# Kernel optimization log

Hardware: AMD Instinct MI355X
Metric: run time of the kernel (lower is better)

## Reference

```python
import jax, jax.numpy as jnp
import numpy as np

SCALE = 8
NUM_CLASSES = 15
IGNORE_THRES = 0.5
# anchors for scale=8 divided by scale
GRID_ANCHOR = jnp.array([[96.0 / 8, 230.0 / 8], [79.0 / 8, 186.0 / 8], [81.0 / 8, 133.0 / 8]], dtype=jnp.float32)  # [3,2]


def _bce_sum(p, t, mask):
    # torch BCELoss(reduction='sum') with log clamped at -100, restricted to mask
    lp = jnp.maximum(jnp.log(p), -100.0)
    ln = jnp.maximum(jnp.log(1.0 - p), -100.0)
    return jnp.sum(-(t * lp + (1.0 - t) * ln) * mask)


def setup_inputs() -> dict:
    key = jax.random.key(0)
    k1, k2, k3 = jax.random.split(key, 3)
    nB, nG = 128, 52
    x = jax.random.normal(k1, (nB, 3 * (NUM_CLASSES + 5), nG, nG), dtype=jnp.float32)
    boxes = jax.random.uniform(k2, (nB, 4), minval=0.1, maxval=0.6)  # cx,cy,w,h in (0,1)
    cls = jax.random.randint(k3, (nB, 1), 0, NUM_CLASSES).astype(jnp.float32)
    labels = jnp.concatenate([boxes, cls], axis=-1)  # [nB,5]
    return {"x": x, "labels": labels}


def reference(x, labels):
    nB, nG = x.shape[0], x.shape[2]
    pred = x.reshape(nB, 3, NUM_CLASSES + 5, nG, nG).transpose(0, 1, 3, 4, 2)  # [B,3,G,G,20]
    px = jax.nn.sigmoid(pred[..., 0])
    py = jax.nn.sigmoid(pred[..., 1])
    pw = pred[..., 2]
    ph = pred[..., 3]
    conf = jax.nn.sigmoid(pred[..., 4])
    cls = jax.nn.softmax(pred[..., 5:], axis=-1)
    pred_boxs = jnp.stack([px, py, pw, ph], axis=-1)  # [B,3,G,G,4]
    out = jnp.concatenate([
        pred_boxs.reshape(nB, -1, 4) * SCALE,
        conf.reshape(nB, -1, 1),
        cls.reshape(nB, -1, NUM_CLASSES),
    ], axis=-1)

    # ---- build_targets (vectorized; one target per image as in original loop) ----
    tb = labels[:, :4] * nG  # boxes in grid units [B,4]
    gx, gy, gw, gh = tb[:, 0], tb[:, 1], tb[:, 2], tb[:, 3]
    gi = gx.astype(jnp.int32)
    gj = gy.astype(jnp.int32)
    gcls = labels[:, 4].astype(jnp.int32)

    # wh-IoU anchors vs targets -> [3,B]
    aw, ah = GRID_ANCHOR[:, 0:1], GRID_ANCHOR[:, 1:2]
    inter_wh = jnp.minimum(aw, gw[None, :]) * jnp.minimum(ah, gh[None, :])
    ious = inter_wh / (aw * ah + 1e-16 + gw[None, :] * gh[None, :] - inter_wh)
    best_idx = jnp.argmax(ious, axis=0)  # [B]

    bidx = jnp.arange(nB)
    shape4 = (nB, 3, nG, nG)
    obj = jnp.zeros(shape4, jnp.float32).at[bidx, best_idx, gj, gi].set(1.0)

    noobj = jnp.ones(shape4, jnp.float32)
    arep = jnp.tile(jnp.arange(3), nB)
    brep = jnp.repeat(bidx, 3)
    jrep = jnp.repeat(gj, 3)
    irep = jnp.repeat(gi, 3)
    ign = (jnp.reshape(ious.T, (-1,)) > IGNORE_THRES).astype(jnp.float32)
    noobj = noobj.at[brep, arep, jrep, irep].mul(1.0 - ign)
    noobj = noobj.at[bidx, best_idx, gj, gi].set(0.0)

    gif = gi.astype(jnp.float32)
    gjf = gj.astype(jnp.float32)
    tx = jnp.zeros(shape4, jnp.float32).at[bidx, best_idx, gj, gi].set(gx - gif)
    ty = jnp.zeros(shape4, jnp.float32).at[bidx, best_idx, gj, gi].set(gy - gjf)
    tw = jnp.zeros(shape4, jnp.float32).at[bidx, best_idx, gj, gi].set(jnp.log(gw / GRID_ANCHOR[best_idx, 0] + 1e-16))
    th = jnp.zeros(shape4, jnp.float32).at[bidx, best_idx, gj, gi].set(jnp.log(gh / GRID_ANCHOR[best_idx, 1] + 1e-16))
    tcls = jnp.zeros(shape4 + (NUM_CLASSES,), jnp.float32).at[bidx, best_idx, gj, gi, gcls].set(1.0)

    # cls_mask: does argmax of predicted class at target cell match gt class
    pred_cls_at = cls[bidx, best_idx, gj, gi]  # [B,15]
    cls_hit = (jnp.argmax(pred_cls_at, axis=-1) == gcls).astype(jnp.float32)
    cls_mask = jnp.zeros(shape4, jnp.float32).at[bidx, best_idx, gj, gi].set(cls_hit)

    # iou between pred box at target cell and target box (cxcywh, +1 corner convention)
    pb = pred_boxs[bidx, best_idx, gj, gi]  # [B,4]
    b1x1, b1y1 = pb[:, 0] - pb[:, 2] / 2, pb[:, 1] - pb[:, 3] / 2
    b1x2, b1y2 = pb[:, 0] + pb[:, 2] / 2, pb[:, 1] + pb[:, 3] / 2
    b2x1, b2y1 = gx - gw / 2, gy - gh / 2
    b2x2, b2y2 = gx + gw / 2, gy + gh / 2
    iw = jnp.clip(jnp.minimum(b1x2, b2x2) - jnp.maximum(b1x1, b2x1) + 1, 0)
    ih = jnp.clip(jnp.minimum(b1y2, b2y2) - jnp.maximum(b1y1, b2y1) + 1, 0)
    inter = iw * ih
    a1 = (b1x2 - b1x1 + 1) * (b1y2 - b1y1 + 1)
    a2 = (b2x2 - b2x1 + 1) * (b2y2 - b2y1 + 1)
    iou_vec = inter / (a1 + a2 - inter + 1e-16)
    iou_scores = jnp.zeros(shape4, jnp.float32).at[bidx, best_idx, gj, gi].set(iou_vec)

    tconf = obj
    # ---- losses (boolean-mask indexing replaced by masked sums) ----
    loss_x = jnp.sum(jnp.abs(px - tx) * obj)
    loss_y = jnp.sum(jnp.abs(py - ty) * obj)
    loss_w = jnp.sum(jnp.abs(pw - tw) * obj)
    loss_h = jnp.sum(jnp.abs(ph - th) * obj)
    loss_conf = _bce_sum(conf, tconf, obj) + 100.0 * _bce_sum(conf, tconf, noobj)
    loss_cls = _bce_sum(cls, tcls, obj[..., None])
    loss = loss_x + loss_y + loss_w + loss_h + loss_conf + loss_cls
    return (loss, out)
```

## Files before the change

kernel.cpp:

```cpp
#include <hip/hip_runtime.h>
#include <math.h>

#define NB    128
#define NG    52
#define NGG   2704
#define NA    3
#define NCLS  15
#define NCH   20
#define NQ    8112
#define TOTAL 1038336
#define BLK   256
#define CPT   2
#define CPB   (BLK*CPT)
#define NBLK  (TOTAL/CPB)
#define FPB   (CPB*NCH)
#define NQUAD ((FPB-4)/4)

__global__ __launch_bounds__(BLK) void main_kernel(const float* __restrict__ x,
                                                   float* __restrict__ out,
                                                   float* __restrict__ partials) {
    __shared__ __align__(16) float sm[FPB];
    __shared__ float wred[BLK/64];

    int t = threadIdx.x;
    int g = blockIdx.x * BLK + t;
    int cell0 = g * CPT;
    int b  = cell0 / NQ;
    int r  = cell0 - b * NQ;
    int a  = r / NGG;
    int ji = r - a * NGG;

    const float2* __restrict__ xp =
        (const float2*)(x + ((size_t)(b*60 + a*20)) * NGG) + (ji >> 1);

    float za[NCH], zb[NCH];
    #pragma unroll
    for (int c = 0; c < NCH; c++) {
        float2 zz = xp[c * (NGG/2)];
        za[c] = zz.x; zb[c] = zz.y;
    }

    float tsum = 0.0f;
    #pragma unroll
    for (int i = 0; i < CPT; i++) {
        const float* z = (i == 0) ? za : zb;
        float v[NCH];
        float conf = 1.0f / (1.0f + expf(-z[4]));
        v[0] = 8.0f / (1.0f + expf(-z[0]));
        v[1] = 8.0f / (1.0f + expf(-z[1]));
        v[2] = 8.0f * z[2];
        v[3] = 8.0f * z[3];
        v[4] = conf;
        float m = z[5];
        #pragma unroll
        for (int c = 6; c < NCH; c++) m = fmaxf(m, z[c]);
        float s = 0.0f;
        #pragma unroll
        for (int c = 0; c < NCLS; c++) { v[5+c] = expf(z[5+c] - m); s += v[5+c]; }
        float inv = 1.0f / s;
        #pragma unroll
        for (int c = 0; c < NCLS; c++) v[5+c] *= inv;

        tsum += -fmaxf(logf(1.0f - conf), -100.0f);

        int cl = (t * CPT + i);
        int base = cl * NCH - 3;
        #pragma unroll
        for (int c = 0; c < NCH; c++) {
            int L = base + c;
            if (L < 0) L += FPB;
            sm[L] = v[c];
        }
    }

    #pragma unroll
    for (int off = 32; off > 0; off >>= 1) tsum += __shfl_down(tsum, off, 64);
    if ((t & 63) == 0) wred[t >> 6] = tsum;

    __syncthreads();

    size_t gbase = (size_t)blockIdx.x * FPB;
    float4* __restrict__ op = (float4*)(out + gbase + 4);
    const float4* __restrict__ sp = (const float4*)sm;
    #pragma unroll
    for (int k = 0; k < 10; k++) {
        int q = k * BLK + t;
        if (q < NQUAD) op[q] = sp[q];
    }
    if (t == 0) {
        out[gbase + 1]    = sm[FPB - 3];
        out[gbase + 2]    = sm[FPB - 2];
        out[gbase + 3]    = sm[FPB - 1];
        out[gbase + FPB]  = sm[FPB - 4];
        partials[blockIdx.x] = wred[0] + wred[1] + wred[2] + wred[3];
    }
}

__global__ void finish_kernel(const float* __restrict__ labels,
                              const float* __restrict__ partials,
                              float* __restrict__ out) {
    int t = threadIdx.x;
    float s = 0.0f;
    for (int q = t; q < NBLK; q += 256) s += partials[q];

    float corr_part = 0.0f;
    if (t < NB) {
        int b = t;
        float gx = labels[b*5+0] * (float)NG;
        float gy = labels[b*5+1] * (float)NG;
        float gw = labels[b*5+2] * (float)NG;
        float gh = labels[b*5+3] * (float)NG;
        int gcls = (int)labels[b*5+4];
        int gi = (int)gx, gj = (int)gy;
        const float aw[3] = {12.0f, 9.875f, 10.125f};
        const float ah[3] = {28.75f, 23.25f, 16.625f};
        float iou[3];
        #pragma unroll
        for (int a = 0; a < 3; a++) {
            float inter = fminf(aw[a], gw) * fminf(ah[a], gh);
            iou[a] = inter / (aw[a]*ah[a] + 1e-16f + gw*gh - inter);
        }
        int best = 0; float bv = iou[0];
        if (iou[1] > bv) { best = 1; bv = iou[1]; }
        if (iou[2] > bv) { best = 2; bv = iou[2]; }
        float txv = gx - (float)gi;
        float tyv = gy - (float)gj;
        float twv = logf(gw / aw[best] + 1e-16f);
        float thv = logf(gh / ah[best] + 1e-16f);

        float corr = 0.0f;
        #pragma unroll
        for (int a = 0; a < 3; a++) {
            int q = a*NGG + gj*NG + gi;
            const float* ob = out + 1 + ((size_t)b*NQ + q) * NCH;
            float conf = ob[4];
            bool isbest = (a == best);
            if (isbest || iou[a] > 0.5f) {
                corr += -fmaxf(logf(1.0f - conf), -100.0f);
            }
            if (isbest) {
                corr_part += -fmaxf(logf(conf), -100.0f);
                float px = ob[0]*0.125f, py = ob[1]*0.125f;
                float pw = ob[2]*0.125f, ph = ob[3]*0.125f;
                corr_part += fabsf(px - txv) + fabsf(py - tyv)
                           + fabsf(pw - twv) + fabsf(ph - thv);
                for (int c = 0; c < NCLS; c++) {
                    float p = ob[5 + c];
                    if (c == gcls) corr_part += -fmaxf(logf(p),        -100.0f);
                    else           corr_part += -fmaxf(logf(1.0f - p), -100.0f);
                }
            }
        }
        corr_part -= 100.0f * corr;
    }

    __shared__ float red[256];
    red[t] = 100.0f * s + corr_part;
    __syncthreads();
    for (int s2 = 128; s2 > 0; s2 >>= 1) {
        if (t < s2) red[t] += red[t + s2];
        __syncthreads();
    }
    if (t == 0) out[0] = red[0];
}

extern "C" void kernel_launch(void* const* d_in, const int* in_sizes, int n_in,
                              void* d_out, int out_size, void* d_ws, size_t ws_size,
                              hipStream_t stream) {
    const float* x      = (const float*)d_in[0];
    const float* labels = (const float*)d_in[1];
    float* out = (float*)d_out;
    float* ws  = (float*)d_ws;

    hipLaunchKernelGGL(main_kernel,   dim3(NBLK), dim3(BLK), 0, stream, x, out, ws);
    hipLaunchKernelGGL(finish_kernel, dim3(1),    dim3(256), 0, stream, labels, ws, out);
}
```

Measured before the change: 157.3 us.

## Write output directly from registers using lane shuffles instead of LDS staging

```diff
diff --git a/kernel.cpp b/kernel.cpp
--- a/kernel.cpp
+++ b/kernel.cpp
@@ -10,21 +10,18 @@
 #define NQ    8112
 #define TOTAL 1038336
 #define BLK   256
-#define CPT   2
-#define CPB   (BLK*CPT)
-#define NBLK  (TOTAL/CPB)
-#define FPB   (CPB*NCH)
-#define NQUAD ((FPB-4)/4)
+#define NTHREADS (TOTAL/2)
+#define NBLK  (NTHREADS/BLK)
+#define NPART (NBLK*4)
+
+__device__ __forceinline__ float sigmoidf(float z) { return 1.0f / (1.0f + expf(-z)); }
 
 __global__ __launch_bounds__(BLK) void main_kernel(const float* __restrict__ x,
                                                    float* __restrict__ out,
                                                    float* __restrict__ partials) {
-    __shared__ __align__(16) float sm[FPB];
-    __shared__ float wred[BLK/64];
-
     int t = threadIdx.x;
-    int g = blockIdx.x * BLK + t;
-    int cell0 = g * CPT;
+    int T = blockIdx.x * BLK + t;
+    int cell0 = T * 2;
     int b  = cell0 / NQ;
     int r  = cell0 - b * NQ;
     int a  = r / NGG;
@@ -40,60 +37,82 @@
         za[c] = zz.x; zb[c] = zz.y;
     }
 
-    float tsum = 0.0f;
-    #pragma unroll
-    for (int i = 0; i < CPT; i++) {
-        const float* z = (i == 0) ? za : zb;
-        float v[NCH];
-        float conf = 1.0f / (1.0f + expf(-z[4]));
-        v[0] = 8.0f / (1.0f + expf(-z[0]));
-        v[1] = 8.0f / (1.0f + expf(-z[1]));
-        v[2] = 8.0f * z[2];
-        v[3] = 8.0f * z[3];
-        v[4] = conf;
-        float m = z[5];
+    float w[40];
+    float tsum;
+
+    float va0 = 8.0f * sigmoidf(za[0]);
+    float va1 = 8.0f * sigmoidf(za[1]);
+    float va2 = 8.0f * za[2];
+    w[0] = 8.0f * za[3];
+    {
+        float conf = sigmoidf(za[4]);
+        w[1] = conf;
+        tsum = -fmaxf(logf(1.0f - conf), -100.0f);
+        float m = za[5];
         #pragma unroll
-        for (int c = 6; c < NCH; c++) m = fmaxf(m, z[c]);
+        for (int c = 6; c < NCH; c++) m = fmaxf(m, za[c]);
         float s = 0.0f;
         #pragma unroll
-        for (int c = 0; c < NCLS; c++) { v[5+c] = expf(z[5+c] - m); s += v[5+c]; }
+        for (int c = 0; c < NCLS; c++) { w[2+c] = expf(za[5+c] - m); s += w[2+c]; }
         float inv = 1.0f / s;
         #pragma unroll
-        for (int c = 0; c < NCLS; c++) v[5+c] *= inv;
+        for (int c = 0; c < NCLS; c++) w[2+c] *= inv;
+    }
 
+    w[17] = 8.0f * sigmoidf(zb[0]);
+    w[18] = 8.0f * sigmoidf(zb[1]);
+    w[19] = 8.0f * zb[2];
+    w[20] = 8.0f * zb[3];
+    {
+        float conf = sigmoidf(zb[4]);
+        w[21] = conf;
         tsum += -fmaxf(logf(1.0f - conf), -100.0f);
+        float m = zb[5];
+        #pragma unroll
+        for (int c = 6; c < NCH; c++) m = fmaxf(m, zb[c]);
+        float s = 0.0f;
+        #pragma unroll
+        for (int c = 0; c < NCLS; c++) { w[22+c] = expf(zb[5+c] - m); s += w[22+c]; }
+        float inv = 1.0f / s;
+        #pragma unroll
+        for (int c = 0; c < NCLS; c++) w[22+c] *= inv;
+    }
 
-        int cl = (t * CPT + i);
-        int base = cl * NCH - 3;
-        #pragma unroll
-        for (int c = 0; c < NCH; c++) {
-            int L = base + c;
-            if (L < 0) L += FPB;
-            sm[L] = v[c];
+    w[37] = __shfl_down(va0, 1, 64);
+    w[38] = __shfl_down(va1, 1, 64);
+    w[39] = __shfl_down(va2, 1, 64);
+    if ((t & 63) == 63) {
+        int cell2 = cell0 + 2;
+        if (cell2 < TOTAL) {
+            int b2  = cell2 / NQ;
+            int r2  = cell2 - b2 * NQ;
+            int a2  = r2 / NGG;
+            int ji2 = r2 - a2 * NGG;
+            const float* q = x + ((size_t)(b2*60 + a2*20)) * NGG + ji2;
+            float z0 = q[0], z1 = q[(size_t)NGG], z2 = q[(size_t)2*NGG];
+            w[37] = 8.0f * sigmoidf(z0);
+            w[38] = 8.0f * sigmoidf(z1);
+            w[39] = 8.0f * z2;
         }
     }
 
+    size_t W = 4 + (size_t)T * 40;
+    float4* __restrict__ op = (float4*)(out + W);
+    if (T != NTHREADS - 1) {
+        #pragma unroll
+        for (int k = 0; k < 10; k++)
+            op[k] = make_float4(w[4*k], w[4*k+1], w[4*k+2], w[4*k+3]);
+    } else {
+        #pragma unroll
+        for (int k = 0; k < 9; k++)
+            op[k] = make_float4(w[4*k], w[4*k+1], w[4*k+2], w[4*k+3]);
+        out[W + 36] = w[36];
+    }
+    if (T == 0) { out[1] = va0; out[2] = va1; out[3] = va2; }
+
     #pragma unroll
     for (int off = 32; off > 0; off >>= 1) tsum += __shfl_down(tsum, off, 64);
-    if ((t & 63) == 0) wred[t >> 6] = tsum;
-
-    __syncthreads();
-
-    size_t gbase = (size_t)blockIdx.x * FPB;
-    float4* __restrict__ op = (float4*)(out + gbase + 4);
-    const float4* __restrict__ sp = (const float4*)sm;
-    #pragma unroll
-    for (int k = 0; k < 10; k++) {
-        int q = k * BLK + t;
-        if (q < NQUAD) op[q] = sp[q];
-    }
-    if (t == 0) {
-        out[gbase + 1]    = sm[FPB - 3];
-        out[gbase + 2]    = sm[FPB - 2];
-        out[gbase + 3]    = sm[FPB - 1];
-        out[gbase + FPB]  = sm[FPB - 4];
-        partials[blockIdx.x] = wred[0] + wred[1] + wred[2] + wred[3];
-    }
+    if ((t & 63) == 0) partials[blockIdx.x * 4 + (t >> 6)] = tsum;
 }
 
 __global__ void finish_kernel(const float* __restrict__ labels,
@@ -101,7 +120,7 @@
                               float* __restrict__ out) {
     int t = threadIdx.x;
     float s = 0.0f;
-    for (int q = t; q < NBLK; q += 256) s += partials[q];
+    for (int q = t; q < NPART; q += 256) s += partials[q];
 
     float corr_part = 0.0f;
     if (t < NB) {
```

Result: slower. 172.7 us (+9.8%).

## Process one cell per thread with padded LDS rows and fast intrinsics

Applied to the files above, without the earlier changes.

```diff
diff --git a/kernel.cpp b/kernel.cpp
--- a/kernel.cpp
+++ b/kernel.cpp
@@ -10,89 +10,80 @@
 #define NQ    8112
 #define TOTAL 1038336
 #define BLK   256
-#define CPT   2
-#define CPB   (BLK*CPT)
-#define NBLK  (TOTAL/CPB)
-#define FPB   (CPB*NCH)
+#define NBLK  (TOTAL/BLK)
+#define FPB   (BLK*NCH)
 #define NQUAD ((FPB-4)/4)
+#define STRIDE 21
+#define NPART (NBLK*4)
+
+__device__ __forceinline__ float fsig(float z) {
+    return __builtin_amdgcn_rcpf(1.0f + __expf(-z));
+}
 
 __global__ __launch_bounds__(BLK) void main_kernel(const float* __restrict__ x,
                                                    float* __restrict__ out,
                                                    float* __restrict__ partials) {
-    __shared__ __align__(16) float sm[FPB];
-    __shared__ float wred[BLK/64];
+    __shared__ float sm[BLK * STRIDE];
 
     int t = threadIdx.x;
-    int g = blockIdx.x * BLK + t;
-    int cell0 = g * CPT;
-    int b  = cell0 / NQ;
-    int r  = cell0 - b * NQ;
+    int cell = blockIdx.x * BLK + t;
+    int b  = cell / NQ;
+    int r  = cell - b * NQ;
     int a  = r / NGG;
     int ji = r - a * NGG;
 
-    const float2* __restrict__ xp =
-        (const float2*)(x + ((size_t)(b*60 + a*20)) * NGG) + (ji >> 1);
+    const float* __restrict__ xp = x + ((size_t)(b*60 + a*20)) * NGG + ji;
+    float z[NCH];
+    #pragma unroll
+    for (int c = 0; c < NCH; c++) z[c] = xp[(size_t)c * NGG];
 
-    float za[NCH], zb[NCH];
+    float conf = fsig(z[4]);
+    float v0 = 8.0f * fsig(z[0]);
+    float v1 = 8.0f * fsig(z[1]);
+    float v2 = 8.0f * z[2];
+    float v3 = 8.0f * z[3];
+
+    float e[NCLS]; float s = 0.0f;
     #pragma unroll
-    for (int c = 0; c < NCH; c++) {
-        float2 zz = xp[c * (NGG/2)];
-        za[c] = zz.x; zb[c] = zz.y;
-    }
+    for (int c = 0; c < NCLS; c++) { e[c] = __expf(z[5+c]); s += e[c]; }
+    float inv = __builtin_amdgcn_rcpf(s);
 
-    float tsum = 0.0f;
+    float* row = sm + t * STRIDE;
+    row[0] = v0; row[1] = v1; row[2] = v2; row[3] = v3; row[4] = conf;
     #pragma unroll
-    for (int i = 0; i < CPT; i++) {
-        const float* z = (i == 0) ? za : zb;
-        float v[NCH];
-        float conf = 1.0f / (1.0f + expf(-z[4]));
-        v[0] = 8.0f / (1.0f + expf(-z[0]));
-        v[1] = 8.0f / (1.0f + expf(-z[1]));
-        v[2] = 8.0f * z[2];
-        v[3] = 8.0f * z[3];
-        v[4] = conf;
-        float m = z[5];
-        #pragma unroll
-        for (int c = 6; c < NCH; c++) m = fmaxf(m, z[c]);
-        float s = 0.0f;
-        #pragma unroll
-        for (int c = 0; c < NCLS; c++) { v[5+c] = expf(z[5+c] - m); s += v[5+c]; }
-        float inv = 1.0f / s;
-        #pragma unroll
-        for (int c = 0; c < NCLS; c++) v[5+c] *= inv;
+    for (int c = 0; c < NCLS; c++) row[5 + c] = e[c] * inv;
 
-        tsum += -fmaxf(logf(1.0f - conf), -100.0f);
-
-        int cl = (t * CPT + i);
-        int base = cl * NCH - 3;
-        #pragma unroll
-        for (int c = 0; c < NCH; c++) {
-            int L = base + c;
-            if (L < 0) L += FPB;
-            sm[L] = v[c];
-        }
-    }
-
+    float tsum = -fmaxf(__logf(1.0f - conf), -100.0f);
     #pragma unroll
     for (int off = 32; off > 0; off >>= 1) tsum += __shfl_down(tsum, off, 64);
-    if ((t & 63) == 0) wred[t >> 6] = tsum;
+    if ((t & 63) == 0) partials[blockIdx.x * 4 + (t >> 6)] = tsum;
 
     __syncthreads();
 
     size_t gbase = (size_t)blockIdx.x * FPB;
     float4* __restrict__ op = (float4*)(out + gbase + 4);
-    const float4* __restrict__ sp = (const float4*)sm;
     #pragma unroll
-    for (int k = 0; k < 10; k++) {
+    for (int k = 0; k < 5; k++) {
         int q = k * BLK + t;
-        if (q < NQUAD) op[q] = sp[q];
+        if (q < NQUAD) {
+            int f  = 4*q + 3;
+            int cl = f / 20;
+            int cc = f - cl * 20;
+            float r0 = sm[cl*STRIDE + cc];
+            cc++; if (cc == 20) { cc = 0; cl++; }
+            float r1 = sm[cl*STRIDE + cc];
+            cc++; if (cc == 20) { cc = 0; cl++; }
+            float r2 = sm[cl*STRIDE + cc];
+            cc++; if (cc == 20) { cc = 0; cl++; }
+            float r3 = sm[cl*STRIDE + cc];
+            op[q] = make_float4(r0, r1, r2, r3);
+        }
     }
     if (t == 0) {
-        out[gbase + 1]    = sm[FPB - 3];
-        out[gbase + 2]    = sm[FPB - 2];
-        out[gbase + 3]    = sm[FPB - 1];
-        out[gbase + FPB]  = sm[FPB - 4];
-        partials[blockIdx.x] = wred[0] + wred[1] + wred[2] + wred[3];
+        out[gbase + 1]   = sm[0];
+        out[gbase + 2]   = sm[1];
+        out[gbase + 3]   = sm[2];
+        out[gbase + FPB] = sm[255*STRIDE + 19];
     }
 }
 
@@ -101,7 +92,7 @@
                               float* __restrict__ out) {
     int t = threadIdx.x;
     float s = 0.0f;
-    for (int q = t; q < NBLK; q += 256) s += partials[q];
+    for (int q = t; q < NPART; q += 256) s += partials[q];
 
     float corr_part = 0.0f;
     if (t < NB) {
```

Result: slower. 171.1 us (+8.8%).
